# Performance work log

Measured on AMD Instinct MI355X. Metric: run time of the kernel, lower is better.

## Reference

```python
import jax, jax.numpy as jnp
import numpy as np


def setup_inputs() -> dict:
    key = jax.random.key(0)
    k1, k2, k3, k4, k5, k6 = jax.random.split(key, 6)
    B, N, K = 2, 60000, 16
    C_in, C_add, C_mid = 64, 3, 16
    out_features = 128
    in_features = (C_in + C_add) * C_mid  # 1072
    return {
        "input_features": jax.random.normal(k1, (B, N, C_in), dtype=jnp.float32),
        "neighbor_inds": jax.random.randint(k2, (B, N, K), 0, N, dtype=jnp.int32),
        "weightnet": jax.random.normal(k3, (B, N, K, C_mid), dtype=jnp.float32),
        "additional_features": jax.random.normal(k4, (B, N, K, C_add), dtype=jnp.float32),
        "linear_weight": jax.random.normal(k5, (out_features, in_features), dtype=jnp.float32) * 0.03,
        "linear_bias": jax.random.normal(k6, (out_features,), dtype=jnp.float32),
    }


def reference(input_features, neighbor_inds, weightnet, additional_features, linear_weight, linear_bias):
    # Gather neighbor features: [B, N, K, C_in]
    gathered = jax.vmap(lambda feats, idx: feats[idx])(input_features, neighbor_inds)
    # Concat per-neighbor additional features: [B, N, K, C_in + C_add]
    feat = jnp.concatenate([gathered, additional_features], axis=-1)
    # PConv: contract over neighbors K against weightnet -> [B, N, C, M]
    pconv = jnp.einsum('bnkc,bnkm->bncm', feat, weightnet)
    B, N = pconv.shape[0], pconv.shape[1]
    pconv = pconv.reshape(B, N, -1)  # [B, N, (C_in+C_add)*C_mid]
    # Fused linear projection
    return jnp.einsum('bnf,of->bno', pconv, linear_weight) + linear_bias
```

## Files before the change

kernel.cpp:

```cpp
#include <hip/hip_runtime.h>

#define NPTS  60000
#define NBLK  3750
#define FP    1088
#define PSTR  1096

typedef _Float16 f16x4 __attribute__((ext_vector_type(4)));
typedef _Float16 f16x8 __attribute__((ext_vector_type(8)));
typedef float    f32x4 __attribute__((ext_vector_type(4)));

__global__ void __launch_bounds__(256)
cvt_lw_kernel(const float* __restrict__ LW, _Float16* __restrict__ LWh) {
    const int o = blockIdx.x;
    for (int f = threadIdx.x; f < FP; f += 256) {
        const float v = (f < 1072) ? LW[o * 1072 + f] : 0.f;
        LWh[(f >> 5) * (128 * 32) + o * 32 + (f & 31)] = (_Float16)v;
    }
}

struct GRegs {
    float fv[4][4];
    float wv[4];
    float av[4];
};

static __device__ __forceinline__ void issue_gather(
    const float* __restrict__ inF, const float* __restrict__ Wn,
    const float* __restrict__ addF, int bbase, int base_nk,
    int ind_lane, int i, int q, int ml, bool mlo, GRegs& g)
{
    #pragma unroll
    for (int j = 0; j < 4; ++j) {
        const int k   = q * 4 + j;
        const int idx = __shfl(ind_lane, i * 16 + k, 64);
        const float* fp = inF + (bbase + idx) * 64 + ml;
        #pragma unroll
        for (int ct = 0; ct < 4; ++ct)
            g.fv[ct][j] = fp[ct * 16];
        g.wv[j] = Wn[(base_nk + k) * 16 + ml];
        g.av[j] = mlo ? addF[(base_nk + k) * 3 + ml] : 0.f;
    }
}

static __device__ __forceinline__ void compute_point(
    const GRegs& g, _Float16* sProw, int q, int ml, bool mlo)
{
    const f32x4 z4 = {0.f, 0.f, 0.f, 0.f};
    f16x4 aW, bA;
    #pragma unroll
    for (int j = 0; j < 4; ++j) { aW[j] = (_Float16)g.wv[j]; bA[j] = (_Float16)g.av[j]; }

    #pragma unroll
    for (int ct = 0; ct < 4; ++ct) {
        f16x4 bF;
        #pragma unroll
        for (int j = 0; j < 4; ++j) bF[j] = (_Float16)g.fv[ct][j];
        const f32x4 d = __builtin_amdgcn_mfma_f32_16x16x16f16(aW, bF, z4, 0, 0, 0);
        f16x4 dh;
        #pragma unroll
        for (int r = 0; r < 4; ++r) dh[r] = (_Float16)d[r];
        *(f16x4*)&sProw[(ct * 16 + ml) * 16 + q * 4] = dh;
    }
    const f32x4 d = __builtin_amdgcn_mfma_f32_16x16x16f16(aW, bA, z4, 0, 0, 0);
    if (mlo) {
        f16x4 dh;
        #pragma unroll
        for (int r = 0; r < 4; ++r) dh[r] = (_Float16)d[r];
        *(f16x4*)&sProw[(64 + ml) * 16 + q * 4] = dh;
    }
}

__global__ void __launch_bounds__(256, 4)
pconv_linear_mfma(const float* __restrict__ inF,
                  const int*   __restrict__ inds,
                  const float* __restrict__ Wn,
                  const float* __restrict__ addF,
                  const _Float16* __restrict__ LWh,
                  const float* __restrict__ bias,
                  float*       __restrict__ out)
{
    __shared__ __align__(16) _Float16 sP[16 * PSTR];

    const int t    = threadIdx.x;
    const int lane = t & 63;
    const int w    = t >> 6;
    const int q    = lane >> 4;
    const int ml   = lane & 15;
    const bool mlo = (ml < 3);

    const int bid   = blockIdx.x;
    const int b     = bid / NBLK;
    const int n0    = (bid - b * NBLK) * 16;
    const int bbase = b * NPTS;

    const int ind_lane = inds[(bbase + n0 + w * 4) * 16 + lane];

    if (t < 128)
        *(unsigned*)&sP[(t >> 3) * PSTR + 1072 + (t & 7) * 2] = 0u;

    const int nk0 = (bbase + n0 + w * 4) * 16;
    _Float16* sPw = sP + (w * 4) * PSTR;
    GRegs gA, gB;
    issue_gather(inF, Wn, addF, bbase, nk0,      ind_lane, 0, q, ml, mlo, gA);
    issue_gather(inF, Wn, addF, bbase, nk0 + 16, ind_lane, 1, q, ml, mlo, gB);
    compute_point(gA, sPw,            q, ml, mlo);
    issue_gather(inF, Wn, addF, bbase, nk0 + 32, ind_lane, 2, q, ml, mlo, gA);
    compute_point(gB, sPw + PSTR,     q, ml, mlo);
    issue_gather(inF, Wn, addF, bbase, nk0 + 48, ind_lane, 3, q, ml, mlo, gB);
    compute_point(gA, sPw + 2 * PSTR, q, ml, mlo);
    compute_point(gB, sPw + 3 * PSTR, q, ml, mlo);
    __syncthreads();

    const int o0 = w * 32;
    const float bz0 = bias[o0 + ml];
    const float bz1 = bias[o0 + 16 + ml];
    f32x4 acc0 = {0.f, 0.f, 0.f, 0.f};
    f32x4 acc1 = {0.f, 0.f, 0.f, 0.f};
    const _Float16* aP = sP + ml * PSTR + q * 8;
    const _Float16* bP = LWh + (o0 + ml) * 32 + q * 8;

    #pragma unroll 4
    for (int ch = 0; ch < 34; ++ch) {
        f16x8 a  = *(const f16x8*)(aP + ch * 32);
        f16x8 b0 = *(const f16x8*)(bP + ch * 4096);
        f16x8 b1 = *(const f16x8*)(bP + ch * 4096 + 512);
        acc0 = __builtin_amdgcn_mfma_f32_16x16x32_f16(a, b0, acc0, 0, 0, 0);
        acc1 = __builtin_amdgcn_mfma_f32_16x16x32_f16(a, b1, acc1, 0, 0, 0);
    }

    float* obase = out + (bbase + n0 + q * 4) * 128;
    #pragma unroll
    for (int r = 0; r < 4; ++r) {
        obase[r * 128 + o0 + ml]      = acc0[r] + bz0;
        obase[r * 128 + o0 + 16 + ml] = acc1[r] + bz1;
    }
}

extern "C" void kernel_launch(void* const* d_in, const int* in_sizes, int n_in,
                              void* d_out, int out_size, void* d_ws, size_t ws_size,
                              hipStream_t stream)
{
    const float* inF  = (const float*)d_in[0];
    const int*   inds = (const int*)  d_in[1];
    const float* Wn   = (const float*)d_in[2];
    const float* addF = (const float*)d_in[3];
    const float* LW   = (const float*)d_in[4];
    const float* bias = (const float*)d_in[5];
    float* out = (float*)d_out;
    _Float16* LWh = (_Float16*)d_ws;

    cvt_lw_kernel<<<dim3(128), dim3(256), 0, stream>>>(LW, LWh);
    pconv_linear_mfma<<<dim3(2 * NBLK), dim3(256), 0, stream>>>(
        inF, inds, Wn, addF, LWh, bias, out);
}
```

Measured before the change: 383.1 us.

## Use 512-thread blocks with two points per wave and XOR-swizzled LDS layout

Doubles the block to 8 waves, so each wave gathers and computes only two points instead of four, and in the linear stage computes 16 output channels instead of 32. The writes into the shared pconv tile use a swizzled quad index, and the MFMA A-operand reads apply a matching flip, to reduce LDS bank conflicts. The intent is more latency hiding for the irregular gathers through higher wave-level parallelism. In exchange, the per-wave gather-compute software pipelining is dropped and each wave loads the same A tile with half the MFMA work per load, so more LDS reads are spent per FLOP.

```diff
diff --git a/kernel.cpp b/kernel.cpp
--- a/kernel.cpp
+++ b/kernel.cpp
@@ -43,7 +43,7 @@
 }
 
 static __device__ __forceinline__ void compute_point(
-    const GRegs& g, _Float16* sProw, int q, int ml, bool mlo)
+    const GRegs& g, _Float16* sProw, int qsw, int ml, bool mlo)
 {
     const f32x4 z4 = {0.f, 0.f, 0.f, 0.f};
     f16x4 aW, bA;
@@ -59,18 +59,18 @@
         f16x4 dh;
         #pragma unroll
         for (int r = 0; r < 4; ++r) dh[r] = (_Float16)d[r];
-        *(f16x4*)&sProw[(ct * 16 + ml) * 16 + q * 4] = dh;
+        *(f16x4*)&sProw[(ct * 16 + ml) * 16 + qsw * 4] = dh;
     }
     const f32x4 d = __builtin_amdgcn_mfma_f32_16x16x16f16(aW, bA, z4, 0, 0, 0);
     if (mlo) {
         f16x4 dh;
         #pragma unroll
         for (int r = 0; r < 4; ++r) dh[r] = (_Float16)d[r];
-        *(f16x4*)&sProw[(64 + ml) * 16 + q * 4] = dh;
+        *(f16x4*)&sProw[(64 + ml) * 16 + qsw * 4] = dh;
     }
 }
 
-__global__ void __launch_bounds__(256, 4)
+__global__ void __launch_bounds__(512, 8)
 pconv_linear_mfma(const float* __restrict__ inF,
                   const int*   __restrict__ inds,
                   const float* __restrict__ Wn,
@@ -87,53 +87,46 @@
     const int q    = lane >> 4;
     const int ml   = lane & 15;
     const bool mlo = (ml < 3);
+    const int qsw  = q ^ (((ml >> 2) & 1) << 1);
 
     const int bid   = blockIdx.x;
     const int b     = bid / NBLK;
     const int n0    = (bid - b * NBLK) * 16;
     const int bbase = b * NPTS;
 
-    const int ind_lane = inds[(bbase + n0 + w * 4) * 16 + lane];
+    const int ind_lane = inds[(bbase + n0 + w * 2) * 16 + (lane & 31)];
 
-    if (t < 128)
-        *(unsigned*)&sP[(t >> 3) * PSTR + 1072 + (t & 7) * 2] = 0u;
+    if (t < 256)
+        sP[(t >> 4) * PSTR + 1072 + (t & 15)] = (_Float16)0.f;
 
-    const int nk0 = (bbase + n0 + w * 4) * 16;
-    _Float16* sPw = sP + (w * 4) * PSTR;
-    GRegs gA, gB;
-    issue_gather(inF, Wn, addF, bbase, nk0,      ind_lane, 0, q, ml, mlo, gA);
-    issue_gather(inF, Wn, addF, bbase, nk0 + 16, ind_lane, 1, q, ml, mlo, gB);
-    compute_point(gA, sPw,            q, ml, mlo);
-    issue_gather(inF, Wn, addF, bbase, nk0 + 32, ind_lane, 2, q, ml, mlo, gA);
-    compute_point(gB, sPw + PSTR,     q, ml, mlo);
-    issue_gather(inF, Wn, addF, bbase, nk0 + 48, ind_lane, 3, q, ml, mlo, gB);
-    compute_point(gA, sPw + 2 * PSTR, q, ml, mlo);
-    compute_point(gB, sPw + 3 * PSTR, q, ml, mlo);
+    const int nk0 = (bbase + n0 + w * 2) * 16;
+    _Float16* sPw = sP + (w * 2) * PSTR;
+    GRegs g0, g1;
+    issue_gather(inF, Wn, addF, bbase, nk0,      ind_lane, 0, q, ml, mlo, g0);
+    issue_gather(inF, Wn, addF, bbase, nk0 + 16, ind_lane, 1, q, ml, mlo, g1);
+    compute_point(g0, sPw,        qsw, ml, mlo);
+    compute_point(g1, sPw + PSTR, qsw, ml, mlo);
     __syncthreads();
 
-    const int o0 = w * 32;
-    const float bz0 = bias[o0 + ml];
-    const float bz1 = bias[o0 + 16 + ml];
-    f32x4 acc0 = {0.f, 0.f, 0.f, 0.f};
-    f32x4 acc1 = {0.f, 0.f, 0.f, 0.f};
-    const _Float16* aP = sP + ml * PSTR + q * 8;
+    const int o0 = w * 16;
+    const float bz = bias[o0 + ml];
+    f32x4 acc = {0.f, 0.f, 0.f, 0.f};
+    const _Float16* aP = sP + ml * PSTR + (q >> 1) * 16 + (q & 1) * 8;
+    const int flip = (q & 1) ? -8 : 8;
     const _Float16* bP = LWh + (o0 + ml) * 32 + q * 8;
 
     #pragma unroll 4
     for (int ch = 0; ch < 34; ++ch) {
-        f16x8 a  = *(const f16x8*)(aP + ch * 32);
-        f16x8 b0 = *(const f16x8*)(bP + ch * 4096);
-        f16x8 b1 = *(const f16x8*)(bP + ch * 4096 + 512);
-        acc0 = __builtin_amdgcn_mfma_f32_16x16x32_f16(a, b0, acc0, 0, 0, 0);
-        acc1 = __builtin_amdgcn_mfma_f32_16x16x32_f16(a, b1, acc1, 0, 0, 0);
+        const int off = ch * 32 + ((ch & 2) ? flip : 0);
+        f16x8 a = *(const f16x8*)(aP + off);
+        f16x8 b = *(const f16x8*)(bP + ch * 4096);
+        acc = __builtin_amdgcn_mfma_f32_16x16x32_f16(a, b, acc, 0, 0, 0);
     }
 
-    float* obase = out + (bbase + n0 + q * 4) * 128;
+    float* obase = out + (bbase + n0 + q * 4) * 128 + o0 + ml;
     #pragma unroll
-    for (int r = 0; r < 4; ++r) {
-        obase[r * 128 + o0 + ml]      = acc0[r] + bz0;
-        obase[r * 128 + o0 + 16 + ml] = acc1[r] + bz1;
-    }
+    for (int r = 0; r < 4; ++r)
+        obase[r * 128] = acc[r] + bz;
 }
 
 extern "C" void kernel_launch(void* const* d_in, const int* in_sizes, int n_in,
@@ -150,6 +143,6 @@
     _Float16* LWh = (_Float16*)d_ws;
 
     cvt_lw_kernel<<<dim3(128), dim3(256), 0, stream>>>(LW, LWh);
-    pconv_linear_mfma<<<dim3(2 * NBLK), dim3(256), 0, stream>>>(
+    pconv_linear_mfma<<<dim3(2 * NBLK), dim3(512), 0, stream>>>(
         inF, inds, Wn, addF, LWh, bias, out);
 }
```

After: 374.9 us. 2.1% less time.
